# Kernel tuning notes

Measured on AMD Instinct MI355X. Metric: run time of the kernel, lower is better.

The kernel has to match this reference:

```python
import jax, jax.numpy as jnp
import numpy as np

HEADS = 16


def setup_inputs() -> dict:
    key = jax.random.key(0)
    k1, k2, k3 = jax.random.split(key, 3)
    B, N, C = 4, 2048, 1024
    x = jax.random.normal(k1, (B, N, C), dtype=jnp.float32)
    w_qkv = jax.random.normal(k2, (C, 3 * C), dtype=jnp.float32) * (C ** -0.5)
    b_qkv = jnp.zeros((3 * C,), dtype=jnp.float32)
    w_out = jax.random.normal(k3, (C, C), dtype=jnp.float32) * (C ** -0.5)
    b_out = jnp.zeros((C,), dtype=jnp.float32)
    return {"x": x, "w_qkv": w_qkv, "b_qkv": b_qkv, "w_out": w_out, "b_out": b_out}


def reference(x, w_qkv, b_qkv, w_out, b_out):
    # Dropout layers act as identity in eval mode.
    B, N, C = x.shape
    H = HEADS
    Dh = C // H
    scale = Dh ** -0.5
    qkv = x @ w_qkv + b_qkv                        # [B, N, 3C]
    qkv = qkv.reshape(B, N, 3, H, Dh)
    q = qkv[:, :, 0].transpose(0, 2, 1, 3)         # [B, H, N, Dh]
    k = qkv[:, :, 1].transpose(0, 2, 1, 3)
    v = qkv[:, :, 2].transpose(0, 2, 1, 3)
    attn = jnp.einsum('bhnd,bhmd->bhnm', q, k) * scale
    attn = jax.nn.softmax(attn, axis=-1)
    out = jnp.einsum('bhnm,bhmd->bhnd', attn, v)   # [B, H, N, Dh]
    out = out.transpose(0, 2, 1, 3).reshape(B, N, C)
    return out @ w_out + b_out
```

## Files before the change

kernel.cpp:

```cpp
#include <hip/hip_runtime.h>

typedef __attribute__((ext_vector_type(8))) short bf16x8;
typedef __attribute__((ext_vector_type(4))) float f32x4;
typedef __attribute__((ext_vector_type(16))) float f32x16;

__device__ __forceinline__ ushort f2bf(float f) {
  union { float f; unsigned u; } v; v.f = f;
  unsigned r = v.u + 0x7fffu + ((v.u >> 16) & 1u);
  return (ushort)(r >> 16);
}

__device__ __forceinline__ float bf2f(ushort u) {
  union { float f; unsigned u; } v; v.u = (unsigned)u << 16;
  return v.f;
}

__device__ __forceinline__ unsigned cvt_pk_bf16(float lo, float hi) {
  unsigned r;
  asm("v_cvt_pk_bf16_f32 %0, %1, %2" : "=v"(r) : "v"(lo), "v"(hi));
  return r;
}

__device__ __forceinline__ void permlane32_swap(unsigned& x, unsigned& y) {
  asm("v_permlane32_swap_b32 %0, %1" : "+v"(x), "+v"(y));
}

__device__ __forceinline__ void gload_lds16(const void* g, void* l) {
  __builtin_amdgcn_global_load_lds(
      (const __attribute__((address_space(1))) void*)g,
      (__attribute__((address_space(3))) void*)l, 16, 0, 0);
}


__global__ void cvt_f32_bf16(const float* __restrict__ s, ushort* __restrict__ d, int n) {
  int i = (blockIdx.x * blockDim.x + threadIdx.x) * 4;
  int stride = gridDim.x * blockDim.x * 4;
  for (; i < n; i += stride) {
    float4 v = *reinterpret_cast<const float4*>(s + i);
    ushort4 o;
    o.x = f2bf(v.x); o.y = f2bf(v.y); o.z = f2bf(v.z); o.w = f2bf(v.w);
    *reinterpret_cast<ushort4*>(d + i) = o;
  }
}

__global__ void transpose_cvt(const float* __restrict__ src, ushort* __restrict__ dst,
                              int R, int C) {
  __shared__ float tile[32][33];
  int c0 = blockIdx.x * 32, r0 = blockIdx.y * 32;
  int tx = threadIdx.x, ty = threadIdx.y;
  #pragma unroll
  for (int i = 0; i < 32; i += 8)
    tile[ty + i][tx] = src[(size_t)(r0 + ty + i) * C + c0 + tx];
  __syncthreads();
  #pragma unroll
  for (int i = 0; i < 32; i += 8)
    dst[(size_t)(c0 + ty + i) * R + r0 + tx] = f2bf(tile[tx][ty + i]);
}


#define GEMM_STAGE(Ap, Bp, kt)                                                 \
  {                                                                            \
    _Pragma("unroll")                                                          \
    for (int c_ = 0; c_ < 4; ++c_) {                                           \
      const int qq_ = c_ * 256 + tid;                                          \
      const int row_ = qq_ >> 3;                                               \
      const int so_ = ((qq_ & 7) ^ (row_ & 7)) * 8;                            \
      gload_lds16(Ap + (size_t)(bm + row_) * 1024 + (kt) + so_,                \
                  (char*)sA + qq_ * 16);                                       \
      gload_lds16(Bp + (size_t)(bn + row_) * 1024 + (kt) + so_,                \
                  (char*)sB + qq_ * 16);                                       \
    }                                                                          \
  }

#define GEMM_COMPUTE()                                                         \
  {                                                                            \
    bf16x8 af[4][2], bfr[4][2];                                                \
    _Pragma("unroll")                                                          \
    for (int mi = 0; mi < 4; ++mi) {                                           \
      const int row_ = wr * 64 + mi * 16 + lr;                                 \
      const char* p_ = (const char*)sA + row_ * 128;                           \
      const int sw_ = (row_ & 7) << 4;                                         \
      af[mi][0] = *(const bf16x8*)(p_ + ((lg * 16) ^ sw_));                    \
      af[mi][1] = *(const bf16x8*)(p_ + ((64 + lg * 16) ^ sw_));               \
    }                                                                          \
    _Pragma("unroll")                                                          \
    for (int ni = 0; ni < 4; ++ni) {                                           \
      const int row_ = wc * 64 + ni * 16 + lr;                                 \
      const char* p_ = (const char*)sB + row_ * 128;                           \
      const int sw_ = (row_ & 7) << 4;                                         \
      bfr[ni][0] = *(const bf16x8*)(p_ + ((lg * 16) ^ sw_));                   \
      bfr[ni][1] = *(const bf16x8*)(p_ + ((64 + lg * 16) ^ sw_));              \
    }                                                                          \
    _Pragma("unroll")                                                          \
    for (int kk = 0; kk < 2; ++kk)                                             \
      _Pragma("unroll")                                                        \
      for (int mi = 0; mi < 4; ++mi)                                           \
        _Pragma("unroll")                                                      \
        for (int ni = 0; ni < 4; ++ni)                                         \
          acc[mi][ni] = __builtin_amdgcn_mfma_f32_16x16x32_bf16(               \
              af[mi][kk], bfr[ni][kk], acc[mi][ni], 0, 0, 0);                  \
  }

#define GEMM_PROLOG                                                            \
  __shared__ __align__(16) ushort sA[128 * 64];                                \
  __shared__ __align__(16) ushort sB[128 * 64];                                \
  const int tid = threadIdx.x;                                                 \
  const int lane = tid & 63;                                                   \
  const int w = tid >> 6;                                                      \
  const int wr = w >> 1, wc = w & 1;                                           \
  const int lr = lane & 15, lg = lane >> 4;                                    \
  f32x4 acc[4][4] = {};


__global__ __launch_bounds__(256) void gemm_qk(const ushort* __restrict__ A,
                                               const ushort* __restrict__ Bt,
                                               const float* __restrict__ bias,
                                               ushort* __restrict__ q,
                                               ushort* __restrict__ k) {
  GEMM_PROLOG;
  const int bm = blockIdx.y * 128;
  const int bn = blockIdx.x * 128;

  for (int kt = 0; kt < 1024; kt += 64) {
    GEMM_STAGE(A, Bt, kt);
    __syncthreads();
    GEMM_COMPUTE();
    __syncthreads();
  }

  ushort* const dst = (bn < 1024) ? q : k;
  const int cb = bn & 1023;
  #pragma unroll
  for (int mi = 0; mi < 4; ++mi)
    #pragma unroll
    for (int ni = 0; ni < 4; ++ni) {
      const int cq = cb + wc * 64 + ni * 16 + lr;
      const int h = cq >> 6, d = cq & 63;
      const float bb = bias[bn + wc * 64 + ni * 16 + lr];
      #pragma unroll
      for (int r = 0; r < 4; ++r) {
        const int row = bm + wr * 64 + mi * 16 + lg * 4 + r;
        const int b_ = row >> 11, n = row & 2047;
        const int bh = b_ * 16 + h;
        dst[((size_t)bh * 2048 + n) * 64 + d] = f2bf(acc[mi][ni][r] + bb);
      }
    }
}


__global__ __launch_bounds__(256) void gemm_vT(const ushort* __restrict__ A,
                                               const ushort* __restrict__ Bt,
                                               const float* __restrict__ bias,
                                               ushort* __restrict__ vT) {
  GEMM_PROLOG;
  const int bm = blockIdx.y * 128;
  const int bn = blockIdx.x * 128;

  for (int kt = 0; kt < 1024; kt += 64) {
    GEMM_STAGE(A, Bt, kt);
    __syncthreads();
    GEMM_COMPUTE();
    __syncthreads();
  }

  const int b_ = bn >> 11, n0 = bn & 2047;
  #pragma unroll
  for (int mi = 0; mi < 4; ++mi)
    #pragma unroll
    for (int ni = 0; ni < 4; ++ni) {
      const int ncol = wc * 64 + ni * 16 + lr;
      #pragma unroll
      for (int r = 0; r < 4; ++r) {
        const int m = wr * 64 + mi * 16 + lg * 4 + r;
        const int vc = bm + m;
        const int h = vc >> 6, d = vc & 63;
        const int bh = b_ * 16 + h;
        const float bb = bias[vc];
        vT[((size_t)bh * 64 + d) * 2048 + n0 + ncol] = f2bf(acc[mi][ni][r] + bb);
      }
    }
}


__global__ __launch_bounds__(256) void gemm_out(const ushort* __restrict__ A,
                                                const ushort* __restrict__ Bt,
                                                const float* __restrict__ bias,
                                                float* __restrict__ out) {
  GEMM_PROLOG;
  const int bm = blockIdx.y * 128;
  const int bn = blockIdx.x * 128;

  for (int kt = 0; kt < 1024; kt += 64) {
    GEMM_STAGE(A, Bt, kt);
    __syncthreads();
    GEMM_COMPUTE();
    __syncthreads();
  }

  #pragma unroll
  for (int mi = 0; mi < 4; ++mi)
    #pragma unroll
    for (int ni = 0; ni < 4; ++ni) {
      const int col = bn + wc * 64 + ni * 16 + lr;
      const float bb = bias[col];
      #pragma unroll
      for (int r = 0; r < 4; ++r) {
        const int row = bm + wr * 64 + mi * 16 + lg * 4 + r;
        out[(size_t)row * 1024 + col] = acc[mi][ni][r] + bb;
      }
    }
}


__global__ __launch_bounds__(512, 2) void attn_fwd(const ushort* __restrict__ q,
                                                   const ushort* __restrict__ k,
                                                   const ushort* __restrict__ vT,
                                                   ushort* __restrict__ o) {
  __shared__ __align__(16) ushort sK[2][64 * 64];
  __shared__ __align__(16) ushort sV[2][64 * 64];

  const int tid = threadIdx.x, lane = tid & 63, w = tid >> 6;
  const int id = blockIdx.x;
  const int xcd = id & 7, j = id >> 3;
  const int bh = xcd * 8 + (j & 7);
  const int qx = j >> 3;
  const int qrow0 = qx * 256 + w * 32;

  const ushort* Qb = q + (size_t)bh * 2048 * 64;
  const ushort* Kb = k + (size_t)bh * 2048 * 64;
  const ushort* Vb = vT + (size_t)bh * 64 * 2048;
  const int lq = lane & 31, hi = lane >> 5;

  const int srow = lane >> 3;
  const int ssw = ((lane & 7) ^ srow) * 8;
  const int krow = w * 8 + srow;

  gload_lds16(Kb + (size_t)krow * 64 + ssw, &sK[0][w * 512]);
  gload_lds16(Vb + (size_t)krow * 2048 + 0 + ssw, &sV[0][w * 512]);

  const float qs = 0.125f * 1.44269504f;
  bf16x8 qf[4];
  #pragma unroll
  for (int dk = 0; dk < 4; ++dk) {
    bf16x8 t = *(const bf16x8*)(Qb + (size_t)(qrow0 + lq) * 64 + dk * 16 + hi * 8);
    #pragma unroll
    for (int jj = 0; jj < 8; ++jj)
      t[jj] = (short)f2bf(bf2f((ushort)t[jj]) * qs);
    qf[dk] = t;
  }

  float m_run = -1e30f, l_run = 0.f;
  f32x16 oacc[2] = {};

  for (int t = 0; t < 32; ++t) {
    const int cur = t & 1;
    if (t + 1 < 32) {
      const int kv2 = (t + 1) << 6;
      gload_lds16(Kb + (size_t)(kv2 + krow) * 64 + ssw, &sK[cur ^ 1][w * 512]);
      gload_lds16(Vb + (size_t)krow * 2048 + kv2 + ssw, &sV[cur ^ 1][w * 512]);
      asm volatile("s_waitcnt vmcnt(2)" ::: "memory");
    } else {
      asm volatile("s_waitcnt vmcnt(0)" ::: "memory");
    }
    __builtin_amdgcn_s_barrier();
    __builtin_amdgcn_sched_barrier(0);

    const char* kb_ = (const char*)&sK[cur][0];
    const char* vb_ = (const char*)&sV[cur][0];

    f32x16 S[2] = {};
    __builtin_amdgcn_s_setprio(1);
    #pragma unroll
    for (int kvt = 0; kvt < 2; ++kvt) {
      const int row = kvt * 32 + lq;
      const int rsw = (row & 7) << 4;
      #pragma unroll
      for (int dk = 0; dk < 4; ++dk) {
        bf16x8 kf = *(const bf16x8*)(kb_ + row * 128 + ((dk * 32 + hi * 16) ^ rsw));
        S[kvt] = __builtin_amdgcn_mfma_f32_32x32x16_bf16(kf, qf[dk], S[kvt], 0, 0, 0);
      }
    }
    __builtin_amdgcn_s_setprio(0);

    float mx = S[0][0];
    #pragma unroll
    for (int kvt = 0; kvt < 2; ++kvt)
      #pragma unroll
      for (int r = 0; r < 16; ++r) mx = fmaxf(mx, S[kvt][r]);
    const float rm = fmaxf(mx, __shfl_xor(mx, 32, 64));

    if (!__all(rm <= m_run + 8.f)) {
      const float mnew = fmaxf(m_run, rm);
      const float corr = __builtin_amdgcn_exp2f(m_run - mnew);
      m_run = mnew;
      l_run *= corr;
      float cq[16];
      #pragma unroll
      for (int r = 0; r < 16; ++r)
        cq[r] = __shfl(corr, (r & 3) + 8 * (r >> 2) + 4 * hi, 64);
      #pragma unroll
      for (int dt = 0; dt < 2; ++dt)
        #pragma unroll
        for (int r = 0; r < 16; ++r) oacc[dt][r] *= cq[r];
    }

    float psum = 0.f;
    unsigned pk_[2][8];
    #pragma unroll
    for (int kvt = 0; kvt < 2; ++kvt) {
      float e[16];
      #pragma unroll
      for (int r = 0; r < 16; ++r) {
        e[r] = __builtin_amdgcn_exp2f(S[kvt][r] - m_run);
        psum += e[r];
      }
      #pragma unroll
      for (int g = 0; g < 4; ++g) {
        pk_[kvt][g * 2 + 0] = cvt_pk_bf16(e[4 * g + 0], e[4 * g + 1]);
        pk_[kvt][g * 2 + 1] = cvt_pk_bf16(e[4 * g + 2], e[4 * g + 3]);
      }
    }
    psum += __shfl_xor(psum, 32, 64);
    l_run += psum;

    __builtin_amdgcn_s_setprio(1);
    #pragma unroll
    for (int kvt = 0; kvt < 2; ++kvt)
      #pragma unroll
      for (int cc = 0; cc < 2; ++cc) {
        unsigned x0 = pk_[kvt][4 * cc + 0], x1 = pk_[kvt][4 * cc + 1];
        unsigned y0 = pk_[kvt][4 * cc + 2], y1 = pk_[kvt][4 * cc + 3];
        permlane32_swap(x0, y0);
        permlane32_swap(x1, y1);
        union { unsigned u[4]; bf16x8 v; } Am;
        Am.u[0] = x0; Am.u[1] = x1; Am.u[2] = y0; Am.u[3] = y1;
        const int cg = kvt * 2 + cc;
        #pragma unroll
        for (int dt = 0; dt < 2; ++dt) {
          const int row = dt * 32 + lq;
          bf16x8 vf = *(const bf16x8*)(vb_ + row * 128 + ((cg * 32 + hi * 16) ^ ((row & 7) << 4)));
          oacc[dt] = __builtin_amdgcn_mfma_f32_32x32x16_bf16(Am.v, vf, oacc[dt], 0, 0, 0);
        }
      }
    __builtin_amdgcn_s_setprio(0);
    __builtin_amdgcn_s_barrier();
  }

  const int b_ = bh >> 4, h = bh & 15;
  float lf[16];
  #pragma unroll
  for (int r = 0; r < 16; ++r)
    lf[r] = __builtin_amdgcn_rcpf(__shfl(l_run, (r & 3) + 8 * (r >> 2) + 4 * hi, 64));
  #pragma unroll
  for (int dt = 0; dt < 2; ++dt)
    #pragma unroll
    for (int r = 0; r < 16; ++r) {
      const int n = qrow0 + (r & 3) + 8 * (r >> 2) + 4 * hi;
      o[(((size_t)b_ * 2048 + n) * 16 + h) * 64 + dt * 32 + lq] = f2bf(oacc[dt][r] * lf[r]);
    }
}


extern "C" void kernel_launch(void* const* d_in, const int* in_sizes, int n_in,
                              void* d_out, int out_size, void* d_ws, size_t ws_size,
                              hipStream_t stream) {
  const float* x = (const float*)d_in[0];
  const float* w_qkv = (const float*)d_in[1];
  const float* b_qkv = (const float*)d_in[2];
  const float* w_out = (const float*)d_in[3];
  const float* b_out = (const float*)d_in[4];
  float* out = (float*)d_out;
  char* ws = (char*)d_ws;

  ushort* xb    = (ushort*)(ws);
  ushort* wqkvT = (ushort*)(ws + 16777216);
  ushort* woutT = (ushort*)(ws + 23068672);
  ushort* qb    = (ushort*)(ws + 25165824);
  ushort* kb    = (ushort*)(ws + 41943040);
  ushort* vTb   = (ushort*)(ws + 58720256);
  ushort* attnb = (ushort*)(ws + 75497472);

  cvt_f32_bf16<<<2048, 256, 0, stream>>>(x, xb, 8192 * 1024);
  transpose_cvt<<<dim3(96, 32), dim3(32, 8), 0, stream>>>(w_qkv, wqkvT, 1024, 3072);
  transpose_cvt<<<dim3(32, 32), dim3(32, 8), 0, stream>>>(w_out, woutT, 1024, 1024);
  gemm_qk<<<dim3(16, 64), 256, 0, stream>>>(xb, wqkvT, b_qkv, qb, kb);
  gemm_vT<<<dim3(64, 8), 256, 0, stream>>>(wqkvT + 2048 * 1024, xb, b_qkv + 2048, vTb);
  attn_fwd<<<512, 512, 0, stream>>>(qb, kb, vTb, attnb);
  gemm_out<<<dim3(8, 64), 256, 0, stream>>>(attnb, woutT, b_out, out);
}
```

Baseline: 196.5 us.

## Double-buffer GEMM LDS tiles and remap blocks for XCD-local L2 reuse

The three projection GEMMs now use two LDS buffers, so the global-to-LDS load for the next K tile is issued before computing on the current one. This replaces the two barriers per iteration with one explicit vmcnt wait plus a barrier. Launch grids become 1D, and block IDs are remapped so that blocks landing on the same XCD work on neighbouring row tiles, which is meant to improve L2 reuse. LDS use per block doubles to 64KB, which may lower occupancy.

Measured after the change: 195.8 us. Within noise of the previous version (-0.3%).

```diff
diff --git a/kernel.cpp b/kernel.cpp
--- a/kernel.cpp
+++ b/kernel.cpp
@@ -58,7 +58,7 @@
 }
 
 
-#define GEMM_STAGE(Ap, Bp, kt)                                                 \
+#define GEMM_STAGE(buf, Ap, Bp, kt)                                            \
   {                                                                            \
     _Pragma("unroll")                                                          \
     for (int c_ = 0; c_ < 4; ++c_) {                                           \
@@ -66,19 +66,21 @@
       const int row_ = qq_ >> 3;                                               \
       const int so_ = ((qq_ & 7) ^ (row_ & 7)) * 8;                            \
       gload_lds16(Ap + (size_t)(bm + row_) * 1024 + (kt) + so_,                \
-                  (char*)sA + qq_ * 16);                                       \
+                  (char*)sA + (buf) * 16384 + qq_ * 16);                       \
       gload_lds16(Bp + (size_t)(bn + row_) * 1024 + (kt) + so_,                \
-                  (char*)sB + qq_ * 16);                                       \
+                  (char*)sB + (buf) * 16384 + qq_ * 16);                       \
     }                                                                          \
   }
 
-#define GEMM_COMPUTE()                                                         \
+#define GEMM_COMPUTE(buf)                                                      \
   {                                                                            \
+    const char* bA_ = (const char*)sA + (buf) * 16384;                         \
+    const char* bB_ = (const char*)sB + (buf) * 16384;                         \
     bf16x8 af[4][2], bfr[4][2];                                                \
     _Pragma("unroll")                                                          \
     for (int mi = 0; mi < 4; ++mi) {                                           \
       const int row_ = wr * 64 + mi * 16 + lr;                                 \
-      const char* p_ = (const char*)sA + row_ * 128;                           \
+      const char* p_ = bA_ + row_ * 128;                                       \
       const int sw_ = (row_ & 7) << 4;                                         \
       af[mi][0] = *(const bf16x8*)(p_ + ((lg * 16) ^ sw_));                    \
       af[mi][1] = *(const bf16x8*)(p_ + ((64 + lg * 16) ^ sw_));               \
@@ -86,7 +88,7 @@
     _Pragma("unroll")                                                          \
     for (int ni = 0; ni < 4; ++ni) {                                           \
       const int row_ = wc * 64 + ni * 16 + lr;                                 \
-      const char* p_ = (const char*)sB + row_ * 128;                           \
+      const char* p_ = bB_ + row_ * 128;                                       \
       const int sw_ = (row_ & 7) << 4;                                         \
       bfr[ni][0] = *(const bf16x8*)(p_ + ((lg * 16) ^ sw_));                   \
       bfr[ni][1] = *(const bf16x8*)(p_ + ((64 + lg * 16) ^ sw_));              \
@@ -101,9 +103,22 @@
               af[mi][kk], bfr[ni][kk], acc[mi][ni], 0, 0, 0);                  \
   }
 
+#define GEMM_PIPELINE(Ap, Bp)                                                  \
+  GEMM_STAGE(0, Ap, Bp, 0);                                                    \
+  asm volatile("s_waitcnt vmcnt(0)" ::: "memory");                             \
+  __builtin_amdgcn_s_barrier();                                                \
+  __builtin_amdgcn_sched_barrier(0);                                           \
+  for (int T = 0; T < 16; ++T) {                                               \
+    if (T + 1 < 16) GEMM_STAGE((T + 1) & 1, Ap, Bp, (T + 1) * 64);             \
+    GEMM_COMPUTE(T & 1);                                                       \
+    asm volatile("s_waitcnt vmcnt(0)" ::: "memory");                           \
+    __builtin_amdgcn_s_barrier();                                              \
+    __builtin_amdgcn_sched_barrier(0);                                         \
+  }
+
 #define GEMM_PROLOG                                                            \
-  __shared__ __align__(16) ushort sA[128 * 64];                                \
-  __shared__ __align__(16) ushort sB[128 * 64];                                \
+  __shared__ __align__(16) ushort sA[2][128 * 64];                             \
+  __shared__ __align__(16) ushort sB[2][128 * 64];                             \
   const int tid = threadIdx.x;                                                 \
   const int lane = tid & 63;                                                   \
   const int w = tid >> 6;                                                      \
@@ -118,15 +133,14 @@
                                                ushort* __restrict__ q,
                                                ushort* __restrict__ k) {
   GEMM_PROLOG;
-  const int bm = blockIdx.y * 128;
-  const int bn = blockIdx.x * 128;
-
-  for (int kt = 0; kt < 1024; kt += 64) {
-    GEMM_STAGE(A, Bt, kt);
-    __syncthreads();
-    GEMM_COMPUTE();
-    __syncthreads();
-  }
+  const int id = blockIdx.x;
+  const int xcd = id & 7, j = id >> 3;
+  const int by = xcd * 8 + (j & 7);
+  const int bx = j >> 3;
+  const int bm = by * 128;
+  const int bn = bx * 128;
+
+  GEMM_PIPELINE(A, Bt);
 
   ushort* const dst = (bn < 1024) ? q : k;
   const int cb = bn & 1023;
@@ -153,15 +167,14 @@
                                                const float* __restrict__ bias,
                                                ushort* __restrict__ vT) {
   GEMM_PROLOG;
-  const int bm = blockIdx.y * 128;
-  const int bn = blockIdx.x * 128;
-
-  for (int kt = 0; kt < 1024; kt += 64) {
-    GEMM_STAGE(A, Bt, kt);
-    __syncthreads();
-    GEMM_COMPUTE();
-    __syncthreads();
-  }
+  const int id = blockIdx.x;
+  const int xcd = id & 7, j = id >> 3;
+  const int bnb = xcd * 8 + (j & 7);
+  const int bmb = j >> 3;
+  const int bm = bmb * 128;
+  const int bn = bnb * 128;
+
+  GEMM_PIPELINE(A, Bt);
 
   const int b_ = bn >> 11, n0 = bn & 2047;
   #pragma unroll
@@ -187,15 +200,14 @@
                                                 const float* __restrict__ bias,
                                                 float* __restrict__ out) {
   GEMM_PROLOG;
-  const int bm = blockIdx.y * 128;
-  const int bn = blockIdx.x * 128;
-
-  for (int kt = 0; kt < 1024; kt += 64) {
-    GEMM_STAGE(A, Bt, kt);
-    __syncthreads();
-    GEMM_COMPUTE();
-    __syncthreads();
-  }
+  const int id = blockIdx.x;
+  const int xcd = id & 7, j = id >> 3;
+  const int by = xcd * 8 + (j & 7);
+  const int bx = j >> 3;
+  const int bm = by * 128;
+  const int bn = bx * 128;
+
+  GEMM_PIPELINE(A, Bt);
 
   #pragma unroll
   for (int mi = 0; mi < 4; ++mi)
@@ -383,8 +395,8 @@
   cvt_f32_bf16<<<2048, 256, 0, stream>>>(x, xb, 8192 * 1024);
   transpose_cvt<<<dim3(96, 32), dim3(32, 8), 0, stream>>>(w_qkv, wqkvT, 1024, 3072);
   transpose_cvt<<<dim3(32, 32), dim3(32, 8), 0, stream>>>(w_out, woutT, 1024, 1024);
-  gemm_qk<<<dim3(16, 64), 256, 0, stream>>>(xb, wqkvT, b_qkv, qb, kb);
-  gemm_vT<<<dim3(64, 8), 256, 0, stream>>>(wqkvT + 2048 * 1024, xb, b_qkv + 2048, vTb);
+  gemm_qk<<<1024, 256, 0, stream>>>(xb, wqkvT, b_qkv, qb, kb);
+  gemm_vT<<<512, 256, 0, stream>>>(wqkvT + 2048 * 1024, xb, b_qkv + 2048, vTb);
   attn_fwd<<<512, 512, 0, stream>>>(qb, kb, vTb, attnb);
-  gemm_out<<<dim3(8, 64), 256, 0, stream>>>(attnb, woutT, b_out, out);
-}
+  gemm_out<<<512, 256, 0, stream>>>(attnb, woutT, b_out, out);
+}
```
